# Performance work log

Hardware: AMD Instinct MI355X
Metric: run time of the kernel (lower is better)

## Reference

```python
import jax, jax.numpy as jnp
import numpy as np

EPS = 0.1

def _kernels():
    # torch: sobel = [[-0.5,0,0.5]]*3 (2D), repeated along depth -> [1,1,3,3,3]
    s = np.array([[-0.5, 0.0, 0.5]] * 3, dtype=np.float32)        # grad along W
    kx = np.tile(s[None, :, :], (3, 1, 1))                        # [3,3,3]
    ky = np.tile(s.T[None, :, :], (3, 1, 1))                      # grad along H
    kz = np.zeros((3, 3, 3), dtype=np.float32)
    kz[0, :, :] = -0.5
    kz[2, :, :] = 0.5                                             # grad along D
    # OIDHW, O=I=1 (channel=1 depthwise)
    return (jnp.asarray(kx)[None, None], jnp.asarray(ky)[None, None], jnp.asarray(kz)[None, None])

KX, KY, KZ = _kernels()

def _conv(x, k):
    return jax.lax.conv_general_dilated(
        x, k, window_strides=(1, 1, 1), padding='VALID',
        dimension_numbers=('NCDHW', 'OIDHW', 'NCDHW'))

def _grads(x):
    # ReplicationPad3d(1) == edge padding on D,H,W
    xp = jnp.pad(x, ((0, 0), (0, 0), (1, 1), (1, 1), (1, 1)), mode='edge')
    return _conv(xp, KX), _conv(xp, KY), _conv(xp, KZ)

def setup_inputs() -> dict:
    key = jax.random.key(0)
    k1, k2, k3 = jax.random.split(key, 3)
    shp = (1, 1, 192, 192, 192)
    return {
        'I': jax.random.normal(k1, shp, dtype=jnp.float32),
        'J': jax.random.normal(k2, shp, dtype=jnp.float32),
        'mask': jax.random.uniform(k3, shp, dtype=jnp.float32),
    }

def reference(I, J, mask):
    Ix, Iy, Iz = _grads(I)
    Jx, Jy, Jz = _grads(J)
    I_mag = Ix * Ix + Iy * Iy + Iz * Iz + EPS * EPS
    J_mag = Jx * Jx + Jy * Jy + Jz * Jz + EPS * EPS
    dot = Ix * Jx + Iy * Jy + Iz * Jz          # == sum over concat channel dim (C=1)
    ngf = (dot * dot) / (I_mag * J_mag)
    return jnp.mean((1.0 - ngf) * mask)
```

## Files before the change

kernel.cpp:

```cpp
#include <hip/hip_runtime.h>

#define NN 192
#define BX 48
#define BZ 4
#define YC 8
#define NTHR (BX * BZ)

struct Raw {
    float4 c[6];
    float  L[6];
    float  R[6];
};

__device__ __forceinline__ void load_plane(const float* const base[6], int yrow,
                                           int dL, int dR, Raw& r) {
#pragma unroll
    for (int d = 0; d < 6; ++d) {
        const float* p = base[d] + yrow;
        r.c[d] = *reinterpret_cast<const float4*>(p);
        r.L[d] = p[dL];
        r.R[d] = p[dR];
    }
}

__device__ __forceinline__ void fold_rows(const float4& cm, float Lm, float Rm,
                                          const float4& c0, float L0, float R0,
                                          const float4& cp, float Lp, float Rp,
                                          float sa[4], float sb[4], float tb[4]) {
    const float wm[6] = {Lm, cm.x, cm.y, cm.z, cm.w, Rm};
    const float w0[6] = {L0, c0.x, c0.y, c0.z, c0.w, R0};
    const float wp[6] = {Lp, cp.x, cp.y, cp.z, cp.w, Rp};
#pragma unroll
    for (int i = 0; i < 4; ++i) {
        const float am = wm[i + 2] - wm[i];
        const float a0 = w0[i + 2] - w0[i];
        const float ap = wp[i + 2] - wp[i];
        const float bm = wm[i] + wm[i + 1] + wm[i + 2];
        const float b0 = w0[i] + w0[i + 1] + w0[i + 2];
        const float bp = wp[i] + wp[i + 1] + wp[i + 2];
        sa[i] = am + a0 + ap;
        sb[i] = bm + b0 + bp;
        tb[i] = bp - bm;
    }
}

__global__ __launch_bounds__(NTHR, 2) void ngf_kernel(const float* __restrict__ I,
                                                      const float* __restrict__ J,
                                                      const float* __restrict__ M,
                                                      float* __restrict__ out) {
    const int tx = threadIdx.x;
    const int tz = threadIdx.y;
    const int x0 = tx * 4;
    const int dL = (tx == 0) ? 0 : -1;
    const int dR = (tx == BX - 1) ? 3 : 4;
    const int z = blockIdx.y * BZ + tz;
    const int ybase = blockIdx.x * YC;

    const int gzm = (z == 0) ? 0 : z - 1;
    const int gzp = (z == NN - 1) ? (NN - 1) : z + 1;

    const float* base[6] = {
        I + gzm * NN * NN + x0, I + z * NN * NN + x0, I + gzp * NN * NN + x0,
        J + gzm * NN * NN + x0, J + z * NN * NN + x0, J + gzp * NN * NN + x0};

    float sa[2][3][4], sb[2][3][4], tb[2][3][4];
    Raw A, B;

    load_plane(base, ((ybase == 0) ? 0 : (ybase - 1)) * NN, dL, dR, A);
    load_plane(base, ybase * NN, dL, dR, B);
    fold_rows(A.c[0], A.L[0], A.R[0], A.c[1], A.L[1], A.R[1], A.c[2], A.L[2], A.R[2],
              sa[0][0], sb[0][0], tb[0][0]);
    fold_rows(A.c[3], A.L[3], A.R[3], A.c[4], A.L[4], A.R[4], A.c[5], A.L[5], A.R[5],
              sa[1][0], sb[1][0], tb[1][0]);
    fold_rows(B.c[0], B.L[0], B.R[0], B.c[1], B.L[1], B.R[1], B.c[2], B.L[2], B.R[2],
              sa[0][1], sb[0][1], tb[0][1]);
    fold_rows(B.c[3], B.L[3], B.R[3], B.c[4], B.L[4], B.R[4], B.c[5], B.L[5], B.R[5],
              sa[1][1], sb[1][1], tb[1][1]);
    load_plane(base, (ybase + 1) * NN, dL, dR, A);
    float4 mcur = *reinterpret_cast<const float4*>(M + (z * NN + ybase) * NN + x0);

    float acc = 0.0f;
#pragma unroll
    for (int yy = 0; yy < YC; ++yy) {
        const int j = yy + 2;
        Raw& cur = (yy & 1) ? B : A;
        Raw& nxt = (yy & 1) ? A : B;

        float4 mnxt = mcur;
        if (yy < YC - 1) {
            int gy = ybase + yy + 2;
            gy = (gy > NN - 1) ? (NN - 1) : gy;
            load_plane(base, gy * NN, dL, dR, nxt);
            mnxt = *reinterpret_cast<const float4*>(M + (z * NN + (ybase + yy + 1)) * NN + x0);
        }

        const int sC = j % 3;
        fold_rows(cur.c[0], cur.L[0], cur.R[0], cur.c[1], cur.L[1], cur.R[1],
                  cur.c[2], cur.L[2], cur.R[2], sa[0][sC], sb[0][sC], tb[0][sC]);
        fold_rows(cur.c[3], cur.L[3], cur.R[3], cur.c[4], cur.L[4], cur.R[4],
                  cur.c[5], cur.L[5], cur.R[5], sa[1][sC], sb[1][sC], tb[1][sC]);

        const int s0 = yy % 3, s1 = (yy + 1) % 3;
        const float mm[4] = {mcur.x, mcur.y, mcur.z, mcur.w};
#pragma unroll
        for (int i = 0; i < 4; ++i) {
            const float Ix = sa[0][s0][i] + sa[0][s1][i] + sa[0][sC][i];
            const float Iy = sb[0][sC][i] - sb[0][s0][i];
            const float Iz = tb[0][s0][i] + tb[0][s1][i] + tb[0][sC][i];
            const float Jx = sa[1][s0][i] + sa[1][s1][i] + sa[1][sC][i];
            const float Jy = sb[1][sC][i] - sb[1][s0][i];
            const float Jz = tb[1][s0][i] + tb[1][s1][i] + tb[1][sC][i];
            const float im = Ix * Ix + Iy * Iy + Iz * Iz + 0.04f;
            const float jm = Jx * Jx + Jy * Jy + Jz * Jz + 0.04f;
            const float dot = Ix * Jx + Iy * Jy + Iz * Jz;
            acc += (1.0f - (dot * dot) / (im * jm)) * mm[i];
        }
        mcur = mnxt;
    }

    acc *= (1.0f / ((float)NN * (float)NN * (float)NN));
#pragma unroll
    for (int off = 32; off > 0; off >>= 1)
        acc += __shfl_down(acc, off, 64);

    __shared__ float red[NTHR / 64];
    const int flat = tz * BX + tx;
    if ((flat & 63) == 0) red[flat >> 6] = acc;
    __syncthreads();
    if (flat == 0) {
        float s = 0.0f;
#pragma unroll
        for (int w = 0; w < NTHR / 64; ++w) s += red[w];
        atomicAdd(out, s);
    }
}

extern "C" void kernel_launch(void* const* d_in, const int* in_sizes, int n_in,
                              void* d_out, int out_size, void* d_ws, size_t ws_size,
                              hipStream_t stream) {
    const float* I = (const float*)d_in[0];
    const float* J = (const float*)d_in[1];
    const float* M = (const float*)d_in[2];
    float* out = (float*)d_out;

    hipMemsetAsync(d_out, 0, sizeof(float), stream);

    dim3 block(BX, BZ);
    dim3 grid(NN / YC, NN / BZ);
    ngf_kernel<<<grid, block, 0, stream>>>(I, J, M, out);
}
```

Baseline: 130.3 us.

## Map one wavefront per x-row with float3 loads and shuffle-based halos

Each x-row of 192 elements is now handled by exactly one 64-lane wavefront, three elements per lane. The left and right neighbours come from cross-lane shuffles instead of extra scalar global loads, which removes the redundant halo loads and the partially filled wavefronts of the old 48-wide blocks. The exact division is also replaced with a hardware reciprocal, which trades a little accuracy for cheaper arithmetic. The float3 loads are less well aligned than the old float4 loads, and the extra shuffles add some instruction overhead.

```diff
diff --git a/kernel.cpp b/kernel.cpp
--- a/kernel.cpp
+++ b/kernel.cpp
@@ -1,58 +1,54 @@
 #include <hip/hip_runtime.h>
 
 #define NN 192
-#define BX 48
 #define BZ 4
 #define YC 8
-#define NTHR (BX * BZ)
+#define NTHR (64 * BZ)
 
-struct Raw {
-    float4 c[6];
-    float  L[6];
-    float  R[6];
-};
 
-__device__ __forceinline__ void load_plane(const float* const base[6], int yrow,
-                                           int dL, int dR, Raw& r) {
+__device__ __forceinline__ void row_ab(float c0, float c1, float c2, int lane,
+                                       float a[3], float b[3]) {
+    float L = __shfl_up(c2, 1, 64);
+    float R = __shfl_down(c0, 1, 64);
+    if (lane == 0)  L = c0;
+    if (lane == 63) R = c2;
+    a[0] = c1 - L;
+    a[1] = c2 - c0;
+    a[2] = R - c1;
+    b[0] = L + c0 + c1;
+    b[1] = c0 + c1 + c2;
+    b[2] = c1 + c2 + R;
+}
+
+__device__ __forceinline__ void fold_plane(const float3 r[3], int lane,
+                                           float sa[3], float sb[3], float tb[3]) {
+    float am[3], bm[3], a0[3], b0[3], ap[3], bp[3];
+    row_ab(r[0].x, r[0].y, r[0].z, lane, am, bm);
+    row_ab(r[1].x, r[1].y, r[1].z, lane, a0, b0);
+    row_ab(r[2].x, r[2].y, r[2].z, lane, ap, bp);
 #pragma unroll
-    for (int d = 0; d < 6; ++d) {
-        const float* p = base[d] + yrow;
-        r.c[d] = *reinterpret_cast<const float4*>(p);
-        r.L[d] = p[dL];
-        r.R[d] = p[dR];
+    for (int i = 0; i < 3; ++i) {
+        sa[i] = am[i] + a0[i] + ap[i];
+        sb[i] = bm[i] + b0[i] + bp[i];
+        tb[i] = bp[i] - bm[i];
     }
 }
 
-__device__ __forceinline__ void fold_rows(const float4& cm, float Lm, float Rm,
-                                          const float4& c0, float L0, float R0,
-                                          const float4& cp, float Lp, float Rp,
-                                          float sa[4], float sb[4], float tb[4]) {
-    const float wm[6] = {Lm, cm.x, cm.y, cm.z, cm.w, Rm};
-    const float w0[6] = {L0, c0.x, c0.y, c0.z, c0.w, R0};
-    const float wp[6] = {Lp, cp.x, cp.y, cp.z, cp.w, Rp};
+__device__ __forceinline__ void load_plane(const float* const base[6], int yrow,
+                                           float3 rI[3], float3 rJ[3]) {
 #pragma unroll
-    for (int i = 0; i < 4; ++i) {
-        const float am = wm[i + 2] - wm[i];
-        const float a0 = w0[i + 2] - w0[i];
-        const float ap = wp[i + 2] - wp[i];
-        const float bm = wm[i] + wm[i + 1] + wm[i + 2];
-        const float b0 = w0[i] + w0[i + 1] + w0[i + 2];
-        const float bp = wp[i] + wp[i + 1] + wp[i + 2];
-        sa[i] = am + a0 + ap;
-        sb[i] = bm + b0 + bp;
-        tb[i] = bp - bm;
-    }
+    for (int d = 0; d < 3; ++d) rI[d] = *reinterpret_cast<const float3*>(base[d] + yrow);
+#pragma unroll
+    for (int d = 0; d < 3; ++d) rJ[d] = *reinterpret_cast<const float3*>(base[3 + d] + yrow);
 }
 
 __global__ __launch_bounds__(NTHR, 2) void ngf_kernel(const float* __restrict__ I,
                                                       const float* __restrict__ J,
                                                       const float* __restrict__ M,
                                                       float* __restrict__ out) {
-    const int tx = threadIdx.x;
+    const int lane = threadIdx.x;
     const int tz = threadIdx.y;
-    const int x0 = tx * 4;
-    const int dL = (tx == 0) ? 0 : -1;
-    const int dR = (tx == BX - 1) ? 3 : 4;
+    const int xoff = lane * 3;
     const int z = blockIdx.y * BZ + tz;
     const int ybase = blockIdx.x * YC;
 
@@ -60,50 +56,47 @@
     const int gzp = (z == NN - 1) ? (NN - 1) : z + 1;
 
     const float* base[6] = {
-        I + gzm * NN * NN + x0, I + z * NN * NN + x0, I + gzp * NN * NN + x0,
-        J + gzm * NN * NN + x0, J + z * NN * NN + x0, J + gzp * NN * NN + x0};
+        I + gzm * NN * NN + xoff, I + z * NN * NN + xoff, I + gzp * NN * NN + xoff,
+        J + gzm * NN * NN + xoff, J + z * NN * NN + xoff, J + gzp * NN * NN + xoff};
+    const float* mbase = M + z * NN * NN + xoff;
 
-    float sa[2][3][4], sb[2][3][4], tb[2][3][4];
-    Raw A, B;
+    float sa[2][3][3], sb[2][3][3], tb[2][3][3];
 
-    load_plane(base, ((ybase == 0) ? 0 : (ybase - 1)) * NN, dL, dR, A);
-    load_plane(base, ybase * NN, dL, dR, B);
-    fold_rows(A.c[0], A.L[0], A.R[0], A.c[1], A.L[1], A.R[1], A.c[2], A.L[2], A.R[2],
-              sa[0][0], sb[0][0], tb[0][0]);
-    fold_rows(A.c[3], A.L[3], A.R[3], A.c[4], A.L[4], A.R[4], A.c[5], A.L[5], A.R[5],
-              sa[1][0], sb[1][0], tb[1][0]);
-    fold_rows(B.c[0], B.L[0], B.R[0], B.c[1], B.L[1], B.R[1], B.c[2], B.L[2], B.R[2],
-              sa[0][1], sb[0][1], tb[0][1]);
-    fold_rows(B.c[3], B.L[3], B.R[3], B.c[4], B.L[4], B.R[4], B.c[5], B.L[5], B.R[5],
-              sa[1][1], sb[1][1], tb[1][1]);
-    load_plane(base, (ybase + 1) * NN, dL, dR, A);
-    float4 mcur = *reinterpret_cast<const float4*>(M + (z * NN + ybase) * NN + x0);
+    {
+        float3 rI[3], rJ[3];
+        load_plane(base, ((ybase == 0) ? 0 : (ybase - 1)) * NN, rI, rJ);
+        fold_plane(rI, lane, sa[0][0], sb[0][0], tb[0][0]);
+        fold_plane(rJ, lane, sa[1][0], sb[1][0], tb[1][0]);
+        load_plane(base, ybase * NN, rI, rJ);
+        fold_plane(rI, lane, sa[0][1], sb[0][1], tb[0][1]);
+        fold_plane(rJ, lane, sa[1][1], sb[1][1], tb[1][1]);
+    }
+
+    float3 bI[2][3], bJ[2][3];
+    load_plane(base, (ybase + 1) * NN, bI[0], bJ[0]);
+    float3 mcur = *reinterpret_cast<const float3*>(mbase + ybase * NN);
 
     float acc = 0.0f;
 #pragma unroll
     for (int yy = 0; yy < YC; ++yy) {
-        const int j = yy + 2;
-        Raw& cur = (yy & 1) ? B : A;
-        Raw& nxt = (yy & 1) ? A : B;
+        const int cb = yy & 1, nb = cb ^ 1;
 
-        float4 mnxt = mcur;
+        float3 mnxt = mcur;
         if (yy < YC - 1) {
             int gy = ybase + yy + 2;
             gy = (gy > NN - 1) ? (NN - 1) : gy;
-            load_plane(base, gy * NN, dL, dR, nxt);
-            mnxt = *reinterpret_cast<const float4*>(M + (z * NN + (ybase + yy + 1)) * NN + x0);
+            load_plane(base, gy * NN, bI[nb], bJ[nb]);
+            mnxt = *reinterpret_cast<const float3*>(mbase + (ybase + yy + 1) * NN);
         }
 
-        const int sC = j % 3;
-        fold_rows(cur.c[0], cur.L[0], cur.R[0], cur.c[1], cur.L[1], cur.R[1],
-                  cur.c[2], cur.L[2], cur.R[2], sa[0][sC], sb[0][sC], tb[0][sC]);
-        fold_rows(cur.c[3], cur.L[3], cur.R[3], cur.c[4], cur.L[4], cur.R[4],
-                  cur.c[5], cur.L[5], cur.R[5], sa[1][sC], sb[1][sC], tb[1][sC]);
+        const int sC = (yy + 2) % 3;
+        fold_plane(bI[cb], lane, sa[0][sC], sb[0][sC], tb[0][sC]);
+        fold_plane(bJ[cb], lane, sa[1][sC], sb[1][sC], tb[1][sC]);
 
         const int s0 = yy % 3, s1 = (yy + 1) % 3;
-        const float mm[4] = {mcur.x, mcur.y, mcur.z, mcur.w};
+        const float mm[3] = {mcur.x, mcur.y, mcur.z};
 #pragma unroll
-        for (int i = 0; i < 4; ++i) {
+        for (int i = 0; i < 3; ++i) {
             const float Ix = sa[0][s0][i] + sa[0][s1][i] + sa[0][sC][i];
             const float Iy = sb[0][sC][i] - sb[0][s0][i];
             const float Iz = tb[0][s0][i] + tb[0][s1][i] + tb[0][sC][i];
@@ -113,7 +106,7 @@
             const float im = Ix * Ix + Iy * Iy + Iz * Iz + 0.04f;
             const float jm = Jx * Jx + Jy * Jy + Jz * Jz + 0.04f;
             const float dot = Ix * Jx + Iy * Jy + Iz * Jz;
-            acc += (1.0f - (dot * dot) / (im * jm)) * mm[i];
+            acc += (1.0f - dot * dot * __builtin_amdgcn_rcpf(im * jm)) * mm[i];
         }
         mcur = mnxt;
     }
@@ -124,7 +117,7 @@
         acc += __shfl_down(acc, off, 64);
 
     __shared__ float red[NTHR / 64];
-    const int flat = tz * BX + tx;
+    const int flat = tz * 64 + lane;
     if ((flat & 63) == 0) red[flat >> 6] = acc;
     __syncthreads();
     if (flat == 0) {
@@ -145,7 +138,7 @@
 
     hipMemsetAsync(d_out, 0, sizeof(float), stream);
 
-    dim3 block(BX, BZ);
+    dim3 block(64, BZ);
     dim3 grid(NN / YC, NN / BZ);
     ngf_kernel<<<grid, block, 0, stream>>>(I, J, M, out);
 }
```

After: 118.4 us. 1.1x faster.
